# Kernel tuning notes

Measured on AMD Instinct MI355X. Metric: run time of the kernel, lower is better.

## Reference

```python
import jax, jax.numpy as jnp
import numpy as np

ND_WEIGHT = 1.0
NUM_CLASS = 1000
B, D = 16384, 2048


def setup_inputs() -> dict:
    key = jax.random.key(0)
    k1, k2, k3, k4 = jax.random.split(key, 4)
    s_emb = jax.random.normal(k1, (B, D), dtype=jnp.float32)
    t_emb = jax.random.normal(k2, (B, D), dtype=jnp.float32)
    T_EMB = jax.random.normal(k3, (NUM_CLASS, D), dtype=jnp.float32)
    labels = jax.random.randint(k4, (B,), 0, NUM_CLASS, dtype=jnp.int64)
    return {"s_emb": s_emb, "t_emb": t_emb, "T_EMB": T_EMB, "labels": labels}


def reference(s_emb, t_emb, T_EMB, labels):
    # Gather per-sample class centers: [B, D]
    centers = T_EMB[labels]
    # Unit-normalize each center (L2 along feature dim)
    e_c = centers / jnp.linalg.norm(centers, axis=-1, keepdims=True)
    # Per-sample max of student/teacher embedding norms: [B]
    s_norm = jnp.linalg.norm(s_emb, axis=-1)
    t_norm = jnp.linalg.norm(t_emb, axis=-1)
    max_norm = jnp.maximum(s_norm, t_norm)
    # 1 - <s, e_c> / max_norm, summed then averaged, scaled by nd_weight
    dots = jnp.sum(s_emb * e_c, axis=-1)
    loss_sum = jnp.sum(1.0 - dots / max_norm)
    return loss_sum * ND_WEIGHT / s_emb.shape[0]
```

## Files before the change

kernel.cpp:

```cpp
#include <hip/hip_runtime.h>


#define NROWS  16384
#define DDIM   2048
#define BLK    256
#define WPB    (BLK / 64)
#define GRID   (NROWS / WPB)

typedef float v4f __attribute__((ext_vector_type(4)));

__global__ __launch_bounds__(BLK, 2) void dnl_main_kernel(
    const float* __restrict__ s_emb,
    const float* __restrict__ t_emb,
    const float* __restrict__ T_EMB,
    const int*   __restrict__ labels,
    float*       __restrict__ partial)
{
    const int tid  = threadIdx.x;
    const int lane = tid & 63;
    const int row  = blockIdx.x * WPB + (tid >> 6);

    const int label = labels[row];

    const v4f* s4 = (const v4f*)(s_emb + (size_t)row   * DDIM);
    const v4f* t4 = (const v4f*)(t_emb + (size_t)row   * DDIM);
    const v4f* c4 = (const v4f*)(T_EMB + (size_t)label * DDIM);

    float ss = 0.f, tt = 0.f, sc = 0.f, cc = 0.f;
    #pragma unroll
    for (int j = 0; j < 8; ++j) {
        const int k = lane + j * 64;
        const v4f s = __builtin_nontemporal_load(&s4[k]);
        const v4f t = __builtin_nontemporal_load(&t4[k]);
        const v4f c = c4[k];
        ss += s.x*s.x + s.y*s.y + s.z*s.z + s.w*s.w;
        tt += t.x*t.x + t.y*t.y + t.z*t.z + t.w*t.w;
        sc += s.x*c.x + s.y*c.y + s.z*c.z + s.w*c.w;
        cc += c.x*c.x + c.y*c.y + c.z*c.z + c.w*c.w;
    }

    #pragma unroll
    for (int off = 32; off > 0; off >>= 1) {
        ss += __shfl_xor(ss, off, 64);
        tt += __shfl_xor(tt, off, 64);
        sc += __shfl_xor(sc, off, 64);
        cc += __shfl_xor(cc, off, 64);
    }

    if (lane == 0) {
        const float max_norm = fmaxf(sqrtf(ss), sqrtf(tt));
        partial[row] = 1.0f - sc / (sqrtf(cc) * max_norm);
    }
}

__global__ __launch_bounds__(BLK) void dnl_reduce_kernel(
    const float* __restrict__ partial,
    float*       __restrict__ out)
{
    const int tid = threadIdx.x;
    const float4* p4 = (const float4*)partial;
    float sum = 0.f;
    #pragma unroll
    for (int j = 0; j < 16; ++j) {
        const float4 v = p4[tid + j * BLK];
        sum += v.x + v.y + v.z + v.w;
    }

    #pragma unroll
    for (int off = 32; off > 0; off >>= 1)
        sum += __shfl_xor(sum, off, 64);

    __shared__ float red[4];
    if ((tid & 63) == 0) red[tid >> 6] = sum;
    __syncthreads();
    if (tid == 0)
        out[0] = (red[0] + red[1] + red[2] + red[3]) * (1.0f / (float)NROWS);
}

__global__ __launch_bounds__(BLK, 2) void dnl_main_atomic_kernel(
    const float* __restrict__ s_emb,
    const float* __restrict__ t_emb,
    const float* __restrict__ T_EMB,
    const int*   __restrict__ labels,
    float*       __restrict__ out)
{
    const int tid  = threadIdx.x;
    const int lane = tid & 63;
    const int row  = blockIdx.x * WPB + (tid >> 6);
    const int label = labels[row];

    const v4f* s4 = (const v4f*)(s_emb + (size_t)row   * DDIM);
    const v4f* t4 = (const v4f*)(t_emb + (size_t)row   * DDIM);
    const v4f* c4 = (const v4f*)(T_EMB + (size_t)label * DDIM);

    float ss = 0.f, tt = 0.f, sc = 0.f, cc = 0.f;
    #pragma unroll
    for (int j = 0; j < 8; ++j) {
        const int k = lane + j * 64;
        const v4f s = __builtin_nontemporal_load(&s4[k]);
        const v4f t = __builtin_nontemporal_load(&t4[k]);
        const v4f c = c4[k];
        ss += s.x*s.x + s.y*s.y + s.z*s.z + s.w*s.w;
        tt += t.x*t.x + t.y*t.y + t.z*t.z + t.w*t.w;
        sc += s.x*c.x + s.y*c.y + s.z*c.z + s.w*c.w;
        cc += c.x*c.x + c.y*c.y + c.z*c.z + c.w*c.w;
    }
    #pragma unroll
    for (int off = 32; off > 0; off >>= 1) {
        ss += __shfl_xor(ss, off, 64);
        tt += __shfl_xor(tt, off, 64);
        sc += __shfl_xor(sc, off, 64);
        cc += __shfl_xor(cc, off, 64);
    }
    if (lane == 0) {
        const float max_norm = fmaxf(sqrtf(ss), sqrtf(tt));
        atomicAdd(out, (1.0f - sc / (sqrtf(cc) * max_norm)) * (1.0f / (float)NROWS));
    }
}

extern "C" void kernel_launch(void* const* d_in, const int* in_sizes, int n_in,
                              void* d_out, int out_size, void* d_ws, size_t ws_size,
                              hipStream_t stream) {
    const float* s_emb  = (const float*)d_in[0];
    const float* t_emb  = (const float*)d_in[1];
    const float* T_EMB  = (const float*)d_in[2];
    const int*   labels = (const int*)d_in[3];
    float* out = (float*)d_out;

    if (ws_size >= (size_t)NROWS * sizeof(float)) {
        float* partial = (float*)d_ws;
        dnl_main_kernel<<<GRID, BLK, 0, stream>>>(s_emb, t_emb, T_EMB, labels, partial);
        dnl_reduce_kernel<<<1, BLK, 0, stream>>>(partial, out);
    } else {
        hipMemsetAsync(d_out, 0, sizeof(float), stream);
        dnl_main_atomic_kernel<<<GRID, BLK, 0, stream>>>(s_emb, t_emb, T_EMB, labels, out);
    }
}
```

Before: 266.2 us.

## Split main kernel into separate s·c and t-norm block groups

The main kernel now launches two kinds of blocks. One group computes s norm, s·c and c norm per row, and a second group computes t squared norms, two rows per wave. Per-row intermediates go to a three-array workspace, and the single-block reduce kernel combines them into the final loss. The aim is to cut per-wave load streams and spread memory traffic over more waves. The cost is extra workspace traffic, a heavier serial reduce, and dependence on the workspace being large enough.

```diff
diff --git a/kernel.cpp b/kernel.cpp
--- a/kernel.cpp
+++ b/kernel.cpp
@@ -5,65 +5,98 @@
 #define DDIM   2048
 #define BLK    256
 #define WPB    (BLK / 64)
-#define GRID   (NROWS / WPB)
+#define SC_BLOCKS (NROWS / WPB)
+#define T_BLOCKS  (NROWS / 2 / WPB)
+#define GRID   (SC_BLOCKS + T_BLOCKS)
 
 typedef float v4f __attribute__((ext_vector_type(4)));
+
+#define WS_DOT 0
+#define WS_SSQ NROWS
+#define WS_TSQ (2 * NROWS)
+#define WS_NEEDED ((size_t)(3 * NROWS) * sizeof(float))
 
 __global__ __launch_bounds__(BLK, 2) void dnl_main_kernel(
     const float* __restrict__ s_emb,
     const float* __restrict__ t_emb,
     const float* __restrict__ T_EMB,
     const int*   __restrict__ labels,
-    float*       __restrict__ partial)
+    float*       __restrict__ ws)
 {
     const int tid  = threadIdx.x;
     const int lane = tid & 63;
-    const int row  = blockIdx.x * WPB + (tid >> 6);
+    const int wib  = tid >> 6;
 
-    const int label = labels[row];
+    float* dot = ws + WS_DOT;
+    float* ssq = ws + WS_SSQ;
+    float* tsq = ws + WS_TSQ;
 
-    const v4f* s4 = (const v4f*)(s_emb + (size_t)row   * DDIM);
-    const v4f* t4 = (const v4f*)(t_emb + (size_t)row   * DDIM);
-    const v4f* c4 = (const v4f*)(T_EMB + (size_t)label * DDIM);
+    if (blockIdx.x < SC_BLOCKS) {
+        const int row   = blockIdx.x * WPB + wib;
+        const int label = labels[row];
 
-    float ss = 0.f, tt = 0.f, sc = 0.f, cc = 0.f;
-    #pragma unroll
-    for (int j = 0; j < 8; ++j) {
-        const int k = lane + j * 64;
-        const v4f s = __builtin_nontemporal_load(&s4[k]);
-        const v4f t = __builtin_nontemporal_load(&t4[k]);
-        const v4f c = c4[k];
-        ss += s.x*s.x + s.y*s.y + s.z*s.z + s.w*s.w;
-        tt += t.x*t.x + t.y*t.y + t.z*t.z + t.w*t.w;
-        sc += s.x*c.x + s.y*c.y + s.z*c.z + s.w*c.w;
-        cc += c.x*c.x + c.y*c.y + c.z*c.z + c.w*c.w;
-    }
+        const v4f* s4 = (const v4f*)(s_emb + (size_t)row   * DDIM);
+        const v4f* c4 = (const v4f*)(T_EMB + (size_t)label * DDIM);
 
-    #pragma unroll
-    for (int off = 32; off > 0; off >>= 1) {
-        ss += __shfl_xor(ss, off, 64);
-        tt += __shfl_xor(tt, off, 64);
-        sc += __shfl_xor(sc, off, 64);
-        cc += __shfl_xor(cc, off, 64);
-    }
+        float ss = 0.f, sc = 0.f, cc = 0.f;
+        #pragma unroll
+        for (int j = 0; j < 8; ++j) {
+            const int k = lane + j * 64;
+            const v4f s = __builtin_nontemporal_load(&s4[k]);
+            const v4f c = c4[k];
+            ss += s.x*s.x + s.y*s.y + s.z*s.z + s.w*s.w;
+            sc += s.x*c.x + s.y*c.y + s.z*c.z + s.w*c.w;
+            cc += c.x*c.x + c.y*c.y + c.z*c.z + c.w*c.w;
+        }
+        #pragma unroll
+        for (int off = 32; off > 0; off >>= 1) {
+            ss += __shfl_xor(ss, off, 64);
+            sc += __shfl_xor(sc, off, 64);
+            cc += __shfl_xor(cc, off, 64);
+        }
+        if (lane == 0) {
+            dot[row] = sc / sqrtf(cc);
+            ssq[row] = ss;
+        }
+    } else {
+        const int i    = (blockIdx.x - SC_BLOCKS) * WPB + wib;
+        const int row0 = 2 * i;
+        const v4f* t4 = (const v4f*)(t_emb + (size_t)row0 * DDIM);
 
-    if (lane == 0) {
-        const float max_norm = fmaxf(sqrtf(ss), sqrtf(tt));
-        partial[row] = 1.0f - sc / (sqrtf(cc) * max_norm);
+        float t0 = 0.f, t1 = 0.f;
+        #pragma unroll
+        for (int j = 0; j < 8; ++j) {
+            const v4f a = __builtin_nontemporal_load(&t4[lane + j * 64]);
+            const v4f b = __builtin_nontemporal_load(&t4[512 + lane + j * 64]);
+            t0 += a.x*a.x + a.y*a.y + a.z*a.z + a.w*a.w;
+            t1 += b.x*b.x + b.y*b.y + b.z*b.z + b.w*b.w;
+        }
+        #pragma unroll
+        for (int off = 32; off > 0; off >>= 1) {
+            t0 += __shfl_xor(t0, off, 64);
+            t1 += __shfl_xor(t1, off, 64);
+        }
+        if (lane == 0) {
+            tsq[row0]     = t0;
+            tsq[row0 + 1] = t1;
+        }
     }
 }
 
 __global__ __launch_bounds__(BLK) void dnl_reduce_kernel(
-    const float* __restrict__ partial,
+    const float* __restrict__ ws,
     float*       __restrict__ out)
 {
     const int tid = threadIdx.x;
-    const float4* p4 = (const float4*)partial;
+    const float* dot = ws + WS_DOT;
+    const float* ssq = ws + WS_SSQ;
+    const float* tsq = ws + WS_TSQ;
+
     float sum = 0.f;
-    #pragma unroll
-    for (int j = 0; j < 16; ++j) {
-        const float4 v = p4[tid + j * BLK];
-        sum += v.x + v.y + v.z + v.w;
+    #pragma unroll 4
+    for (int i = tid; i < NROWS; i += BLK) {
+        const float mn = fmaxf(sqrtf(ssq[i]), sqrtf(tsq[i]));
+        sum += 1.0f - dot[i] / mn;
     }
 
     #pragma unroll
@@ -127,12 +160,13 @@
     const int*   labels = (const int*)d_in[3];
     float* out = (float*)d_out;
 
-    if (ws_size >= (size_t)NROWS * sizeof(float)) {
-        float* partial = (float*)d_ws;
-        dnl_main_kernel<<<GRID, BLK, 0, stream>>>(s_emb, t_emb, T_EMB, labels, partial);
-        dnl_reduce_kernel<<<1, BLK, 0, stream>>>(partial, out);
+    if (ws_size >= WS_NEEDED) {
+        float* ws = (float*)d_ws;
+        dnl_main_kernel<<<GRID, BLK, 0, stream>>>(s_emb, t_emb, T_EMB, labels, ws);
+        dnl_reduce_kernel<<<1, BLK, 0, stream>>>(ws, out);
     } else {
         hipMemsetAsync(d_out, 0, sizeof(float), stream);
-        dnl_main_atomic_kernel<<<GRID, BLK, 0, stream>>>(s_emb, t_emb, T_EMB, labels, out);
+        dnl_main_atomic_kernel<<<NROWS / WPB, BLK, 0, stream>>>(
+            s_emb, t_emb, T_EMB, labels, out);
     }
 }
```

After: 275.8 us. 1.04x slower.
